# Performance work log

Measured on AMD Instinct MI355X. Metric: run time of the kernel, lower is better.

Reference implementation:

```python
import jax, jax.numpy as jnp
import numpy as np

N, E = 100000, 1600000
IN_C, HID, OUT_C = 128, 16, 32
H1, H2 = 8, 8  # heads for conv1/conv2; conv3 has 1 head, concat=False
NEG_SLOPE = 0.2


def setup_inputs() -> dict:
    key = jax.random.key(0)
    ks = jax.random.split(key, 16)
    def p(k, shape, fan_in):
        return jax.random.normal(k, shape, jnp.float32) * (1.0 / np.sqrt(fan_in))
    inp = {
        "x": jax.random.normal(ks[0], (N, IN_C), jnp.float32),
        "edge_index": jax.random.randint(ks[1], (2, E), 0, N, jnp.int32),
        # conv1: in=128 -> heads=8, ch=16, concat
        "W1": p(ks[2], (IN_C, H1 * HID), IN_C),
        "a_src1": p(ks[3], (H1, HID), HID),
        "a_dst1": p(ks[4], (H1, HID), HID),
        "b1": jnp.zeros((H1 * HID,), jnp.float32),
        # conv2: in=128 -> heads=8, ch=16, concat
        "W2": p(ks[5], (H1 * HID, H2 * HID), H1 * HID),
        "a_src2": p(ks[6], (H2, HID), HID),
        "a_dst2": p(ks[7], (H2, HID), HID),
        "b2": jnp.zeros((H2 * HID,), jnp.float32),
        # conv3: in=128 -> heads=1, ch=32, concat=False
        "W3": p(ks[8], (H2 * HID, OUT_C), H2 * HID),
        "a_src3": p(ks[9], (1, OUT_C), OUT_C),
        "a_dst3": p(ks[10], (1, OUT_C), OUT_C),
        "b3": jnp.zeros((OUT_C,), jnp.float32),
    }
    return inp


def gat_conv(x, src, dst, W, a_src, a_dst, b, heads, ch, concat):
    """PyG-style GATConv (eval mode): gather -> leaky_relu -> segment softmax -> scatter sum."""
    n = x.shape[0]
    h = (x @ W).reshape(n, heads, ch)                 # [N, H, C]
    al_s = jnp.sum(h * a_src, axis=-1)                # [N, H] source-side logit part
    al_d = jnp.sum(h * a_dst, axis=-1)                # [N, H] dest-side logit part
    logits = jax.nn.leaky_relu(al_s[src] + al_d[dst], NEG_SLOPE)  # [Etot, H]
    m = jax.ops.segment_max(logits, dst, num_segments=n)         # per-dest max (self loops guarantee >=1 edge)
    e = jnp.exp(logits - m[dst])
    denom = jax.ops.segment_sum(e, dst, num_segments=n)
    alpha = e / denom[dst]                            # [Etot, H]
    msgs = h[src] * alpha[..., None]                  # [Etot, H, C]
    out = jax.ops.segment_sum(msgs, dst, num_segments=n)  # [N, H, C]
    if concat:
        return out.reshape(n, heads * ch) + b
    return out.mean(axis=1) + b


def reference(x, edge_index, W1, a_src1, a_dst1, b1, W2, a_src2, a_dst2, b2,
              W3, a_src3, a_dst3, b3):
    n = x.shape[0]
    loops = jnp.arange(n, dtype=edge_index.dtype)     # PyG add_self_loops=True
    src = jnp.concatenate([edge_index[0], loops])
    dst = jnp.concatenate([edge_index[1], loops])
    h = jax.nn.relu(gat_conv(x, src, dst, W1, a_src1, a_dst1, b1, H1, HID, True))
    h = jax.nn.relu(gat_conv(h, src, dst, W2, a_src2, a_dst2, b2, H2, HID, True))
    h = gat_conv(h, src, dst, W3, a_src3, a_dst3, b3, 1, OUT_C, False)
    # global_mean_pool with all-zero batch vector -> mean over all nodes
    return h.mean(axis=0, keepdims=True)              # [1, OUT_C]
```

## Files before the change

### kernel.cpp

```cpp
#include <hip/hip_runtime.h>


typedef unsigned short bfu;
typedef unsigned char u8;
typedef __attribute__((ext_vector_type(8))) short bf16x8;
typedef __attribute__((ext_vector_type(4))) float f32x4;
typedef __attribute__((ext_vector_type(2))) float f32x2;

constexpr int N_NODES = 100000;
constexpr int E_IN    = 1600000;
constexpr int E_TOT   = E_IN + N_NODES;
constexpr float NEG   = 0.2f;
constexpr int P_XCD   = 8;
constexpr int PSZ     = N_NODES / P_XCD;
constexpr int CAP     = 64;
constexpr int AGG32_B = N_NODES / 32;

__device__ inline bfu f2bf(float f) {
    union { float f; unsigned i; } c; c.f = f;
    unsigned x = c.i;
    return (bfu)((x + 0x7fffu + ((x >> 16) & 1u)) >> 16);
}
__device__ inline u8 f2fp8(float f) {
    return (u8)(__builtin_amdgcn_cvt_pk_fp8_f32(f, f, 0, false) & 0xff);
}


__global__ void fill_csr_part(const int* __restrict__ ei, int* __restrict__ cursor,
                              int* __restrict__ srclist) {
    int p = blockIdx.x & 7;
    int b = blockIdx.x >> 3;
    int lo = p * PSZ, hi = lo + PSZ;
    int e0 = (b * 256 + threadIdx.x) * 4;
    if (e0 >= E_TOT) return;
    bool self = e0 >= E_IN;
    int4 d4;
    if (!self) d4 = *(const int4*)&ei[E_IN + e0];
    else { int bb = e0 - E_IN; d4 = make_int4(bb, bb + 1, bb + 2, bb + 3); }
    int dd[4] = {d4.x, d4.y, d4.z, d4.w};
    #pragma unroll
    for (int q = 0; q < 4; ++q) {
        int d = dd[q];
        if (d >= lo && d < hi) {
            int s = self ? (e0 - E_IN + q) : ei[e0 + q];
            int pos = atomicAdd(&cursor[d], 1);
            if (pos < CAP) srclist[d * CAP + pos] = s;
        }
    }
}


__global__ void transpose_w(const float* __restrict__ W1, const float* __restrict__ W2,
                            const float* __restrict__ W3,
                            bfu* __restrict__ Wt1, bfu* __restrict__ Wt2,
                            bfu* __restrict__ Wt3) {
    int idx = blockIdx.x * 256 + threadIdx.x;
    if (idx < 16384) {
        int k = idx >> 7, n = idx & 127;
        Wt1[n * 128 + k] = f2bf(W1[idx]);
    } else if (idx < 32768) {
        int r = idx - 16384;
        int k = r >> 7, n = r & 127;
        Wt2[n * 128 + k] = f2bf(W2[r]);
    } else if (idx < 32768 + 4096) {
        int r = idx - 32768;
        int k = r >> 5, n = r & 31;
        Wt3[n * 128 + k] = f2bf(W3[r]);
    }
}


__device__ inline bf16x8 ldcvt_f32(const float* p) {
    float4 v0 = *(const float4*)p;
    float4 v1 = *(const float4*)(p + 4);
    bf16x8 a;
    a[0] = (short)f2bf(v0.x); a[1] = (short)f2bf(v0.y);
    a[2] = (short)f2bf(v0.z); a[3] = (short)f2bf(v0.w);
    a[4] = (short)f2bf(v1.x); a[5] = (short)f2bf(v1.y);
    a[6] = (short)f2bf(v1.z); a[7] = (short)f2bf(v1.w);
    return a;
}

template<int COUT, bool F32A, int H>
__global__ __launch_bounds__(256) void gemm_mfma(const void* __restrict__ Xg_,
                                                 const bfu* __restrict__ Wt,
                                                 const float* __restrict__ a_src,
                                                 const float* __restrict__ a_dst,
                                                 u8* __restrict__ Y,
                                                 float* __restrict__ als,
                                                 float* __restrict__ ald) {
    constexpr int NT = COUT / 16;
    int wid  = threadIdx.x >> 6;
    int lane = threadIdx.x & 63;
    int m = lane & 15, quad = lane >> 4;
    int rbase = (blockIdx.x * 4 + wid) * 16;
    if (rbase >= N_NODES) return;
    int rA = rbase + m; if (rA >= N_NODES) rA = N_NODES - 1;

    bf16x8 a0, a1, a2, a3;
    if constexpr (F32A) {
        const float* Ap = (const float*)Xg_ + (size_t)rA * 128 + quad * 8;
        a0 = ldcvt_f32(Ap);
        a1 = ldcvt_f32(Ap + 32);
        a2 = ldcvt_f32(Ap + 64);
        a3 = ldcvt_f32(Ap + 96);
    } else {
        const bfu* Ap = (const bfu*)Xg_ + (size_t)rA * 128 + quad * 8;
        a0 = *(const bf16x8*)(Ap);
        a1 = *(const bf16x8*)(Ap + 32);
        a2 = *(const bf16x8*)(Ap + 64);
        a3 = *(const bf16x8*)(Ap + 96);
    }

    const bfu* Bp = Wt + (size_t)m * 128 + quad * 8;
    f32x4 acc[NT];
    #pragma unroll
    for (int nt = 0; nt < NT; nt++) {
        const bfu* Bn = Bp + nt * 16 * 128;
        f32x4 c = {0.f, 0.f, 0.f, 0.f};
        c = __builtin_amdgcn_mfma_f32_16x16x32_bf16(a0, *(const bf16x8*)(Bn),      c, 0, 0, 0);
        c = __builtin_amdgcn_mfma_f32_16x16x32_bf16(a1, *(const bf16x8*)(Bn + 32), c, 0, 0, 0);
        c = __builtin_amdgcn_mfma_f32_16x16x32_bf16(a2, *(const bf16x8*)(Bn + 64), c, 0, 0, 0);
        c = __builtin_amdgcn_mfma_f32_16x16x32_bf16(a3, *(const bf16x8*)(Bn + 96), c, 0, 0, 0);
        acc[nt] = c;
    }

    #pragma unroll
    for (int nt = 0; nt < NT; nt++) {
        #pragma unroll
        for (int r = 0; r < 4; r++) {
            int row = rbase + quad * 4 + r;
            if (row < N_NODES)
                Y[(size_t)row * COUT + nt * 16 + m] = f2fp8(acc[nt][r]);
        }
    }

    if constexpr (H == 8) {
        #pragma unroll
        for (int nt = 0; nt < NT; nt++) {
            float as_ = a_src[nt * 16 + m];
            float ad_ = a_dst[nt * 16 + m];
            #pragma unroll
            for (int r = 0; r < 4; r++) {
                float vs = acc[nt][r] * as_;
                float vd = acc[nt][r] * ad_;
                #pragma unroll
                for (int mask = 1; mask < 16; mask <<= 1) {
                    vs += __shfl_xor(vs, mask);
                    vd += __shfl_xor(vd, mask);
                }
                int row = rbase + quad * 4 + r;
                if (m == 0 && row < N_NODES) {
                    als[row * 8 + nt] = vs;
                    ald[row * 8 + nt] = vd;
                }
            }
        }
    } else {
        float as0 = a_src[m], as1 = a_src[16 + m];
        float ad0 = a_dst[m], ad1 = a_dst[16 + m];
        #pragma unroll
        for (int r = 0; r < 4; r++) {
            float vs = acc[0][r] * as0 + acc[1][r] * as1;
            float vd = acc[0][r] * ad0 + acc[1][r] * ad1;
            #pragma unroll
            for (int mask = 1; mask < 16; mask <<= 1) {
                vs += __shfl_xor(vs, mask);
                vd += __shfl_xor(vd, mask);
            }
            int row = rbase + quad * 4 + r;
            if (m == 0 && row < N_NODES) {
                als[row] = vs;
                ald[row] = vd;
            }
        }
    }
}


__global__ __launch_bounds__(256) void agg128(const u8* __restrict__ Hb,
        const float* __restrict__ als, const float* __restrict__ ald,
        const int* __restrict__ deg, const int* __restrict__ srclist,
        const float* __restrict__ bias, bfu* __restrict__ out) {
    int wave = (blockIdx.x * 256 + threadIdx.x) >> 6;
    int lane = threadIdx.x & 63;
    int sub  = lane >> 4;
    int li   = lane & 15;
    int d    = wave * 4 + sub;
    if (d >= N_NODES) return;
    int c0 = li * 8;
    int h  = li >> 1;
    float ad = ald[d * 8 + h];
    const int* sl = srclist + d * CAP;
    int n = deg[d];
    float a0=0.f,a1=0.f,a2=0.f,a3=0.f,a4=0.f,a5=0.f,a6=0.f,a7=0.f,den=0.f;
    int j = 0;
    for (; j + 4 <= n; j += 4) {
        int s0 = sl[j], s1 = sl[j+1], s2 = sl[j+2], s3 = sl[j+3];
        uint2 u0 = *(const uint2*)(Hb + (size_t)s0 * 128 + c0);
        uint2 u1 = *(const uint2*)(Hb + (size_t)s1 * 128 + c0);
        uint2 u2 = *(const uint2*)(Hb + (size_t)s2 * 128 + c0);
        uint2 u3 = *(const uint2*)(Hb + (size_t)s3 * 128 + c0);
        float x0 = als[s0*8+h], x1 = als[s1*8+h], x2 = als[s2*8+h], x3 = als[s3*8+h];
        float l0 = x0 + ad; l0 = fmaxf(l0, NEG*l0); float w0 = __expf(l0);
        float l1 = x1 + ad; l1 = fmaxf(l1, NEG*l1); float w1 = __expf(l1);
        float l2 = x2 + ad; l2 = fmaxf(l2, NEG*l2); float w2 = __expf(l2);
        float l3 = x3 + ad; l3 = fmaxf(l3, NEG*l3); float w3 = __expf(l3);
        den += (w0 + w1) + (w2 + w3);
        {
            f32x2 p0 = __builtin_amdgcn_cvt_pk_f32_fp8((int)u0.x, false);
            f32x2 p1 = __builtin_amdgcn_cvt_pk_f32_fp8((int)u0.x, true);
            f32x2 p2 = __builtin_amdgcn_cvt_pk_f32_fp8((int)u0.y, false);
            f32x2 p3 = __builtin_amdgcn_cvt_pk_f32_fp8((int)u0.y, true);
            a0=fmaf(w0,p0[0],a0); a1=fmaf(w0,p0[1],a1); a2=fmaf(w0,p1[0],a2); a3=fmaf(w0,p1[1],a3);
            a4=fmaf(w0,p2[0],a4); a5=fmaf(w0,p2[1],a5); a6=fmaf(w0,p3[0],a6); a7=fmaf(w0,p3[1],a7);
        }
        {
            f32x2 p0 = __builtin_amdgcn_cvt_pk_f32_fp8((int)u1.x, false);
            f32x2 p1 = __builtin_amdgcn_cvt_pk_f32_fp8((int)u1.x, true);
            f32x2 p2 = __builtin_amdgcn_cvt_pk_f32_fp8((int)u1.y, false);
            f32x2 p3 = __builtin_amdgcn_cvt_pk_f32_fp8((int)u1.y, true);
            a0=fmaf(w1,p0[0],a0); a1=fmaf(w1,p0[1],a1); a2=fmaf(w1,p1[0],a2); a3=fmaf(w1,p1[1],a3);
            a4=fmaf(w1,p2[0],a4); a5=fmaf(w1,p2[1],a5); a6=fmaf(w1,p3[0],a6); a7=fmaf(w1,p3[1],a7);
        }
        {
            f32x2 p0 = __builtin_amdgcn_cvt_pk_f32_fp8((int)u2.x, false);
            f32x2 p1 = __builtin_amdgcn_cvt_pk_f32_fp8((int)u2.x, true);
            f32x2 p2 = __builtin_amdgcn_cvt_pk_f32_fp8((int)u2.y, false);
            f32x2 p3 = __builtin_amdgcn_cvt_pk_f32_fp8((int)u2.y, true);
            a0=fmaf(w2,p0[0],a0); a1=fmaf(w2,p0[1],a1); a2=fmaf(w2,p1[0],a2); a3=fmaf(w2,p1[1],a3);
            a4=fmaf(w2,p2[0],a4); a5=fmaf(w2,p2[1],a5); a6=fmaf(w2,p3[0],a6); a7=fmaf(w2,p3[1],a7);
        }
        {
            f32x2 p0 = __builtin_amdgcn_cvt_pk_f32_fp8((int)u3.x, false);
            f32x2 p1 = __builtin_amdgcn_cvt_pk_f32_fp8((int)u3.x, true);
            f32x2 p2 = __builtin_amdgcn_cvt_pk_f32_fp8((int)u3.y, false);
            f32x2 p3 = __builtin_amdgcn_cvt_pk_f32_fp8((int)u3.y, true);
            a0=fmaf(w3,p0[0],a0); a1=fmaf(w3,p0[1],a1); a2=fmaf(w3,p1[0],a2); a3=fmaf(w3,p1[1],a3);
            a4=fmaf(w3,p2[0],a4); a5=fmaf(w3,p2[1],a5); a6=fmaf(w3,p3[0],a6); a7=fmaf(w3,p3[1],a7);
        }
    }
    for (; j < n; ++j) {
        int s0 = sl[j];
        uint2 u0 = *(const uint2*)(Hb + (size_t)s0 * 128 + c0);
        float x0 = als[s0*8+h];
        float l0 = x0 + ad; l0 = fmaxf(l0, NEG*l0); float w0 = __expf(l0);
        den += w0;
        f32x2 p0 = __builtin_amdgcn_cvt_pk_f32_fp8((int)u0.x, false);
        f32x2 p1 = __builtin_amdgcn_cvt_pk_f32_fp8((int)u0.x, true);
        f32x2 p2 = __builtin_amdgcn_cvt_pk_f32_fp8((int)u0.y, false);
        f32x2 p3 = __builtin_amdgcn_cvt_pk_f32_fp8((int)u0.y, true);
        a0=fmaf(w0,p0[0],a0); a1=fmaf(w0,p0[1],a1); a2=fmaf(w0,p1[0],a2); a3=fmaf(w0,p1[1],a3);
        a4=fmaf(w0,p2[0],a4); a5=fmaf(w0,p2[1],a5); a6=fmaf(w0,p3[0],a6); a7=fmaf(w0,p3[1],a7);
    }
    float r = 1.f / den;
    float4 b0 = *(const float4*)&bias[c0];
    float4 b1 = *(const float4*)&bias[c0 + 4];
    float o0 = fmaxf(fmaf(a0, r, b0.x), 0.f);
    float o1 = fmaxf(fmaf(a1, r, b0.y), 0.f);
    float o2 = fmaxf(fmaf(a2, r, b0.z), 0.f);
    float o3 = fmaxf(fmaf(a3, r, b0.w), 0.f);
    float o4 = fmaxf(fmaf(a4, r, b1.x), 0.f);
    float o5 = fmaxf(fmaf(a5, r, b1.y), 0.f);
    float o6 = fmaxf(fmaf(a6, r, b1.z), 0.f);
    float o7 = fmaxf(fmaf(a7, r, b1.w), 0.f);
    uint4 st;
    st.x = (unsigned)f2bf(o0) | ((unsigned)f2bf(o1) << 16);
    st.y = (unsigned)f2bf(o2) | ((unsigned)f2bf(o3) << 16);
    st.z = (unsigned)f2bf(o4) | ((unsigned)f2bf(o5) << 16);
    st.w = (unsigned)f2bf(o6) | ((unsigned)f2bf(o7) << 16);
    *(uint4*)&out[(size_t)d * 128 + c0] = st;
}

__global__ __launch_bounds__(256) void agg32(const u8* __restrict__ Hb,
        const float* __restrict__ als, const float* __restrict__ ald,
        const int* __restrict__ deg, const int* __restrict__ srclist,
        const float* __restrict__ bias, float* __restrict__ outp) {
    __shared__ float lds[4][32];
    int t    = threadIdx.x;
    int wid  = t >> 6;
    int lane = t & 63;
    int sub  = lane >> 3;
    int li   = lane & 7;
    int d    = blockIdx.x * 32 + wid * 8 + sub;
    int c0 = li * 4;
    float adv = ald[d];
    const int* sl = srclist + d * CAP;
    int n = deg[d];
    float a0=0.f,a1=0.f,a2=0.f,a3=0.f,den=0.f;
    int j = 0;
    for (; j + 4 <= n; j += 4) {
        int s0 = sl[j], s1 = sl[j+1], s2 = sl[j+2], s3 = sl[j+3];
        unsigned u0 = *(const unsigned*)(Hb + (size_t)s0 * 32 + c0);
        unsigned u1 = *(const unsigned*)(Hb + (size_t)s1 * 32 + c0);
        unsigned u2 = *(const unsigned*)(Hb + (size_t)s2 * 32 + c0);
        unsigned u3 = *(const unsigned*)(Hb + (size_t)s3 * 32 + c0);
        float x0 = als[s0], x1 = als[s1], x2 = als[s2], x3 = als[s3];
        float l0 = x0 + adv; l0 = fmaxf(l0, NEG*l0); float w0 = __expf(l0);
        float l1 = x1 + adv; l1 = fmaxf(l1, NEG*l1); float w1 = __expf(l1);
        float l2 = x2 + adv; l2 = fmaxf(l2, NEG*l2); float w2 = __expf(l2);
        float l3 = x3 + adv; l3 = fmaxf(l3, NEG*l3); float w3 = __expf(l3);
        den += (w0 + w1) + (w2 + w3);
        f32x2 p;
        p = __builtin_amdgcn_cvt_pk_f32_fp8((int)u0, false); a0=fmaf(w0,p[0],a0); a1=fmaf(w0,p[1],a1);
        p = __builtin_amdgcn_cvt_pk_f32_fp8((int)u0, true);  a2=fmaf(w0,p[0],a2); a3=fmaf(w0,p[1],a3);
        p = __builtin_amdgcn_cvt_pk_f32_fp8((int)u1, false); a0=fmaf(w1,p[0],a0); a1=fmaf(w1,p[1],a1);
        p = __builtin_amdgcn_cvt_pk_f32_fp8((int)u1, true);  a2=fmaf(w1,p[0],a2); a3=fmaf(w1,p[1],a3);
        p = __builtin_amdgcn_cvt_pk_f32_fp8((int)u2, false); a0=fmaf(w2,p[0],a0); a1=fmaf(w2,p[1],a1);
        p = __builtin_amdgcn_cvt_pk_f32_fp8((int)u2, true);  a2=fmaf(w2,p[0],a2); a3=fmaf(w2,p[1],a3);
        p = __builtin_amdgcn_cvt_pk_f32_fp8((int)u3, false); a0=fmaf(w3,p[0],a0); a1=fmaf(w3,p[1],a1);
        p = __builtin_amdgcn_cvt_pk_f32_fp8((int)u3, true);  a2=fmaf(w3,p[0],a2); a3=fmaf(w3,p[1],a3);
    }
    for (; j < n; ++j) {
        int s0 = sl[j];
        unsigned u0 = *(const unsigned*)(Hb + (size_t)s0 * 32 + c0);
        float x0 = als[s0];
        float l0 = x0 + adv; l0 = fmaxf(l0, NEG*l0); float w0 = __expf(l0);
        den += w0;
        f32x2 p;
        p = __builtin_amdgcn_cvt_pk_f32_fp8((int)u0, false); a0=fmaf(w0,p[0],a0); a1=fmaf(w0,p[1],a1);
        p = __builtin_amdgcn_cvt_pk_f32_fp8((int)u0, true);  a2=fmaf(w0,p[0],a2); a3=fmaf(w0,p[1],a3);
    }
    float r = 1.f / den;
    float4 bv = *(const float4*)&bias[c0];
    float o0 = fmaf(a0, r, bv.x), o1 = fmaf(a1, r, bv.y);
    float o2 = fmaf(a2, r, bv.z), o3 = fmaf(a3, r, bv.w);
    #pragma unroll
    for (int mask = 8; mask < 64; mask <<= 1) {
        o0 += __shfl_xor(o0, mask);
        o1 += __shfl_xor(o1, mask);
        o2 += __shfl_xor(o2, mask);
        o3 += __shfl_xor(o3, mask);
    }
    if (sub == 0) {
        lds[wid][c0]     = o0;
        lds[wid][c0 + 1] = o1;
        lds[wid][c0 + 2] = o2;
        lds[wid][c0 + 3] = o3;
    }
    __syncthreads();
    if (t < 32)
        atomicAdd(&outp[t],
            (lds[0][t] + lds[1][t] + lds[2][t] + lds[3][t]) * (1.0f / N_NODES));
}


extern "C" void kernel_launch(void* const* d_in, const int* in_sizes, int n_in,
                              void* d_out, int out_size, void* d_ws, size_t ws_size,
                              hipStream_t stream) {
    (void)in_sizes; (void)n_in; (void)out_size; (void)ws_size;
    const float* x   = (const float*)d_in[0];
    const int*   ei  = (const int*)d_in[1];
    const float* W1  = (const float*)d_in[2];
    const float* as1 = (const float*)d_in[3];
    const float* ad1 = (const float*)d_in[4];
    const float* b1  = (const float*)d_in[5];
    const float* W2  = (const float*)d_in[6];
    const float* as2 = (const float*)d_in[7];
    const float* ad2 = (const float*)d_in[8];
    const float* b2  = (const float*)d_in[9];
    const float* W3  = (const float*)d_in[10];
    const float* as3 = (const float*)d_in[11];
    const float* ad3 = (const float*)d_in[12];
    const float* b3  = (const float*)d_in[13];

    char* ws = (char*)d_ws;
    size_t off = 0;
    auto carve = [&](size_t bytes) { void* p = ws + off; off += (bytes + 255) & ~size_t(255); return p; };
    u8*    bufH    = (u8*)carve(size_t(N_NODES) * 128);
    bfu*   bufF    = (bfu*)carve(size_t(N_NODES) * 128 * 2);
    float* als     = (float*)carve(size_t(N_NODES) * 8 * 4);
    float* ald     = (float*)carve(size_t(N_NODES) * 8 * 4);
    int*   cursor  = (int*)carve(size_t(N_NODES) * 4);
    bfu*   Wt1     = (bfu*)carve(128 * 128 * 2);
    bfu*   Wt2     = (bfu*)carve(128 * 128 * 2);
    bfu*   Wt3     = (bfu*)carve(32 * 128 * 2);
    int*   srclist = (int*)carve(size_t(N_NODES) * CAP * 4);

    const int EDGE_B4 = (E_TOT / 4 + 255) / 256;
    const int GEMM_B  = (N_NODES + 63) / 64;

    hipMemsetAsync(cursor, 0, size_t(N_NODES) * 4, stream);
    hipMemsetAsync(d_out, 0, 32 * 4, stream);

    transpose_w<<<(36864 + 255) / 256, 256, 0, stream>>>(W1, W2, W3, Wt1, Wt2, Wt3);
    fill_csr_part<<<EDGE_B4 * P_XCD, 256, 0, stream>>>(ei, cursor, srclist);

    gemm_mfma<128, true, 8><<<GEMM_B, 256, 0, stream>>>(x, Wt1, as1, ad1, bufH, als, ald);
    agg128<<<(N_NODES + 15) / 16, 256, 0, stream>>>(bufH, als, ald, cursor, srclist, b1, bufF);

    gemm_mfma<128, false, 8><<<GEMM_B, 256, 0, stream>>>(bufF, Wt2, as2, ad2, bufH, als, ald);
    agg128<<<(N_NODES + 15) / 16, 256, 0, stream>>>(bufH, als, ald, cursor, srclist, b2, bufF);

    gemm_mfma<32, false, 1><<<GEMM_B, 256, 0, stream>>>(bufF, Wt3, as3, ad3, bufH, als, ald);
    agg32<<<AGG32_B, 256, 0, stream>>>(bufH, als, ald, cursor, srclist, b3, (float*)d_out);
}
```

Measured before the change: 452.2 us.

## Fuse CSR fill into first GEMM launch with block-index dispatch

Merges the CSR-building edge pass and the first-layer GEMM into one kernel, with the first GEMM_B blocks running the GEMM and the rest running the fill. The two are independent, so they can overlap on the GPU and one launch boundary goes away. The fill also now uses nontemporal loads for edge indices and an unsigned range check for the partition test. Mixing a memory- and atomic-heavy phase with the MFMA phase could cause contention, and block-0 ordering puts the GEMM blocks first.

After: 451.4 us. No clear change (-0.2%).

```diff
diff --git a/kernel.cpp b/kernel.cpp
--- a/kernel.cpp
+++ b/kernel.cpp
@@ -6,6 +6,7 @@
 typedef __attribute__((ext_vector_type(8))) short bf16x8;
 typedef __attribute__((ext_vector_type(4))) float f32x4;
 typedef __attribute__((ext_vector_type(2))) float f32x2;
+typedef __attribute__((ext_vector_type(4))) int i32x4;
 
 constexpr int N_NODES = 100000;
 constexpr int E_IN    = 1600000;
@@ -15,6 +16,9 @@
 constexpr int PSZ     = N_NODES / P_XCD;
 constexpr int CAP     = 64;
 constexpr int AGG32_B = N_NODES / 32;
+constexpr int GEMM_B  = (N_NODES + 63) / 64;
+constexpr int EDGE_B4 = (E_TOT / 4 + 255) / 256;
+constexpr int FILL_B  = EDGE_B4 * P_XCD;
 
 __device__ inline bfu f2bf(float f) {
     union { float f; unsigned i; } c; c.f = f;
@@ -26,23 +30,22 @@
 }
 
 
-__global__ void fill_csr_part(const int* __restrict__ ei, int* __restrict__ cursor,
-                              int* __restrict__ srclist) {
-    int p = blockIdx.x & 7;
-    int b = blockIdx.x >> 3;
-    int lo = p * PSZ, hi = lo + PSZ;
-    int e0 = (b * 256 + threadIdx.x) * 4;
+__device__ inline void fill_body(int g, int tid, const int* __restrict__ ei,
+                                 int* __restrict__ cursor, int* __restrict__ srclist) {
+    int p = g & 7;
+    int b = g >> 3;
+    int lo = p * PSZ;
+    int e0 = (b * 256 + tid) * 4;
     if (e0 >= E_TOT) return;
     bool self = e0 >= E_IN;
-    int4 d4;
-    if (!self) d4 = *(const int4*)&ei[E_IN + e0];
-    else { int bb = e0 - E_IN; d4 = make_int4(bb, bb + 1, bb + 2, bb + 3); }
-    int dd[4] = {d4.x, d4.y, d4.z, d4.w};
+    i32x4 d4;
+    if (!self) d4 = __builtin_nontemporal_load((const i32x4*)(ei + E_IN + e0));
+    else { int bb = e0 - E_IN; d4 = (i32x4){bb, bb + 1, bb + 2, bb + 3}; }
     #pragma unroll
     for (int q = 0; q < 4; ++q) {
-        int d = dd[q];
-        if (d >= lo && d < hi) {
-            int s = self ? (e0 - E_IN + q) : ei[e0 + q];
+        int d = d4[q];
+        if ((unsigned)(d - lo) < (unsigned)PSZ) {
+            int s = self ? (e0 - E_IN + q) : __builtin_nontemporal_load(ei + e0 + q);
             int pos = atomicAdd(&cursor[d], 1);
             if (pos < CAP) srclist[d * CAP + pos] = s;
         }
@@ -82,18 +85,18 @@
 }
 
 template<int COUT, bool F32A, int H>
-__global__ __launch_bounds__(256) void gemm_mfma(const void* __restrict__ Xg_,
-                                                 const bfu* __restrict__ Wt,
-                                                 const float* __restrict__ a_src,
-                                                 const float* __restrict__ a_dst,
-                                                 u8* __restrict__ Y,
-                                                 float* __restrict__ als,
-                                                 float* __restrict__ ald) {
+__device__ inline void gemm_body(int bidx, const void* __restrict__ Xg_,
+                                 const bfu* __restrict__ Wt,
+                                 const float* __restrict__ a_src,
+                                 const float* __restrict__ a_dst,
+                                 u8* __restrict__ Y,
+                                 float* __restrict__ als,
+                                 float* __restrict__ ald) {
     constexpr int NT = COUT / 16;
     int wid  = threadIdx.x >> 6;
     int lane = threadIdx.x & 63;
     int m = lane & 15, quad = lane >> 4;
-    int rbase = (blockIdx.x * 4 + wid) * 16;
+    int rbase = (bidx * 4 + wid) * 16;
     if (rbase >= N_NODES) return;
     int rA = rbase + m; if (rA >= N_NODES) rA = N_NODES - 1;
 
@@ -175,6 +178,29 @@
             }
         }
     }
+}
+
+__global__ __launch_bounds__(256) void gemm1_fill(const float* __restrict__ x,
+        const bfu* __restrict__ Wt1, const float* __restrict__ as1,
+        const float* __restrict__ ad1, u8* __restrict__ Y,
+        float* __restrict__ als, float* __restrict__ ald,
+        const int* __restrict__ ei, int* __restrict__ cursor,
+        int* __restrict__ srclist) {
+    if (blockIdx.x < GEMM_B)
+        gemm_body<128, true, 8>(blockIdx.x, x, Wt1, as1, ad1, Y, als, ald);
+    else
+        fill_body(blockIdx.x - GEMM_B, threadIdx.x, ei, cursor, srclist);
+}
+
+template<int COUT, bool F32A, int H>
+__global__ __launch_bounds__(256) void gemm_mfma(const void* __restrict__ Xg_,
+                                                 const bfu* __restrict__ Wt,
+                                                 const float* __restrict__ a_src,
+                                                 const float* __restrict__ a_dst,
+                                                 u8* __restrict__ Y,
+                                                 float* __restrict__ als,
+                                                 float* __restrict__ ald) {
+    gemm_body<COUT, F32A, H>(blockIdx.x, Xg_, Wt, a_src, a_dst, Y, als, ald);
 }
 
 
@@ -377,16 +403,13 @@
     bfu*   Wt3     = (bfu*)carve(32 * 128 * 2);
     int*   srclist = (int*)carve(size_t(N_NODES) * CAP * 4);
 
-    const int EDGE_B4 = (E_TOT / 4 + 255) / 256;
-    const int GEMM_B  = (N_NODES + 63) / 64;
-
     hipMemsetAsync(cursor, 0, size_t(N_NODES) * 4, stream);
     hipMemsetAsync(d_out, 0, 32 * 4, stream);
 
     transpose_w<<<(36864 + 255) / 256, 256, 0, stream>>>(W1, W2, W3, Wt1, Wt2, Wt3);
-    fill_csr_part<<<EDGE_B4 * P_XCD, 256, 0, stream>>>(ei, cursor, srclist);
-
-    gemm_mfma<128, true, 8><<<GEMM_B, 256, 0, stream>>>(x, Wt1, as1, ad1, bufH, als, ald);
+
+    gemm1_fill<<<GEMM_B + FILL_B, 256, 0, stream>>>(x, Wt1, as1, ad1, bufH, als, ald,
+                                                    ei, cursor, srclist);
     agg128<<<(N_NODES + 15) / 16, 256, 0, stream>>>(bufH, als, ald, cursor, srclist, b1, bufF);
 
     gemm_mfma<128, false, 8><<<GEMM_B, 256, 0, stream>>>(bufF, Wt2, as2, ad2, bufH, als, ald);
```
